# Kernel optimization log

Hardware: AMD Instinct MI355X
Metric: run time of the kernel (lower is better)

## Reference

```python
import jax, jax.numpy as jnp
from jax import lax
import numpy as np

INPUT, HIDDEN, OUTPUT, SEQ = 1024, 1024, 1024, 8192


def setup_inputs() -> dict:
    key = jax.random.key(0)
    ks = jax.random.split(key, 7)
    s = 1.0 / np.sqrt(HIDDEN)
    return {
        "input_seq": jax.random.normal(ks[0], (SEQ, INPUT), dtype=jnp.float32),
        # PyTorch nn.LSTM params, gate order [i, f, g, o]
        "W_ih": jax.random.uniform(ks[1], (4 * HIDDEN, INPUT), jnp.float32, -s, s),
        "W_hh": jax.random.uniform(ks[2], (4 * HIDDEN, HIDDEN), jnp.float32, -s, s),
        "b_ih": jax.random.uniform(ks[3], (4 * HIDDEN,), jnp.float32, -s, s),
        "b_hh": jax.random.uniform(ks[4], (4 * HIDDEN,), jnp.float32, -s, s),
        "W_out": jax.random.uniform(ks[5], (OUTPUT, HIDDEN), jnp.float32, -s, s),
        "b_out": jax.random.uniform(ks[6], (OUTPUT,), jnp.float32, -s, s),
    }


def reference(input_seq, W_ih, W_hh, b_ih, b_hh, W_out, b_out):
    H = W_hh.shape[1]
    # Precompute input projections for all timesteps in one GEMM: [S, 4H]
    x_gates = input_seq @ W_ih.T + (b_ih + b_hh)

    def step(carry, xg):
        h, c = carry
        gates = xg + h @ W_hh.T                      # [4H]
        i = jax.nn.sigmoid(gates[:H])
        f = jax.nn.sigmoid(gates[H:2 * H])
        g = jnp.tanh(gates[2 * H:3 * H])
        o = jax.nn.sigmoid(gates[3 * H:])
        c = f * c + i * g
        h = o * jnp.tanh(c)
        return (h, c), None

    h0 = jnp.zeros((H,), dtype=input_seq.dtype)
    (h_final, _), _ = lax.scan(step, (h0, h0), x_gates)
    # Original applies linear per-timestep then takes predictions[-1];
    # linear is pointwise in time, so projecting only h_final is identical math.
    return h_final @ W_out.T + b_out
```

## Files before the change

### kernel.cpp

```cpp
#include <hip/hip_runtime.h>
#include <hip/hip_fp16.h>

typedef _Float16 h2v __attribute__((ext_vector_type(2)));

__device__ __forceinline__ float fdot2(unsigned int a, unsigned int b, float c) {
    return __builtin_amdgcn_fdot2(__builtin_bit_cast(h2v, a),
                                  __builtin_bit_cast(h2v, b), c, false);
}

#define SCOPE_SYS __HIP_MEMORY_SCOPE_SYSTEM

__global__ __launch_bounds__(256) void k_f2h(const float* __restrict__ src,
                                             __half* __restrict__ dst, int n4) {
    int i = blockIdx.x * 256 + threadIdx.x;
    if (i >= n4) return;
    float4 v = ((const float4*)src)[i];
    union { __half2 h[2]; uint2 u; } o;
    o.h[0] = __halves2half2(__float2half_rn(v.x), __float2half_rn(v.y));
    o.h[1] = __halves2half2(__float2half_rn(v.z), __float2half_rn(v.w));
    ((uint2*)dst)[i] = o.u;
}

__global__ __launch_bounds__(256) void k_bias(const float* __restrict__ a,
                                              const float* __restrict__ b,
                                              float* __restrict__ o) {
    int i = blockIdx.x * 256 + threadIdx.x;
    if (i < 4096) o[i] = a[i] + b[i];
}

__global__ __launch_bounds__(256) void k_gemm_xg(const __half* __restrict__ A,
                                                 const __half* __restrict__ B,
                                                 const float* __restrict__ bias,
                                                 __half* __restrict__ C) {
    __shared__ unsigned int As[128][20];
    __shared__ unsigned int Bs[128][20];
    const int tid = threadIdx.x;
    const int tx = tid & 15, ty = tid >> 4;
    const int m0 = blockIdx.x * 128, n0 = blockIdx.y * 128;
    float acc[8][8];
#pragma unroll
    for (int i = 0; i < 8; ++i)
#pragma unroll
        for (int j = 0; j < 8; ++j) acc[i][j] = 0.f;
    const unsigned int* Ag = (const unsigned int*)(A + (size_t)m0 * 1024);
    const unsigned int* Bg = (const unsigned int*)(B + (size_t)n0 * 1024);
    for (int k0 = 0; k0 < 512; k0 += 16) {
        __syncthreads();
#pragma unroll
        for (int j = 0; j < 2; ++j) {
            int qd = j * 256 + tid;
            int row = qd >> 2;
            int c4 = (qd & 3) << 2;
            uint4 va = *(const uint4*)(Ag + (size_t)row * 512 + k0 + c4);
            uint4 vb = *(const uint4*)(Bg + (size_t)row * 512 + k0 + c4);
            *(uint4*)&As[row][c4] = va;
            *(uint4*)&Bs[row][c4] = vb;
        }
        __syncthreads();
#pragma unroll
        for (int k2 = 0; k2 < 16; k2 += 2) {
            unsigned int a0[8], a1[8], b0[8], b1[8];
#pragma unroll
            for (int i = 0; i < 8; ++i) {
                uint2 v = *(const uint2*)&As[ty + 16 * i][k2];
                a0[i] = v.x; a1[i] = v.y;
            }
#pragma unroll
            for (int j = 0; j < 8; ++j) {
                uint2 v = *(const uint2*)&Bs[tx + 16 * j][k2];
                b0[j] = v.x; b1[j] = v.y;
            }
#pragma unroll
            for (int i = 0; i < 8; ++i)
#pragma unroll
                for (int j = 0; j < 8; ++j) {
                    acc[i][j] = fdot2(a0[i], b0[j], acc[i][j]);
                    acc[i][j] = fdot2(a1[i], b1[j], acc[i][j]);
                }
        }
    }
#pragma unroll
    for (int i = 0; i < 8; ++i) {
        int row = m0 + ty + 16 * i;
#pragma unroll
        for (int j = 0; j < 8; ++j) {
            int col = n0 + tx + 16 * j;
            C[(size_t)row * 4096 + col] = __float2half_rn(acc[i][j] + bias[col]);
        }
    }
}

__global__ __launch_bounds__(512, 1) void k_lstm(const __half* __restrict__ Whh,
                                                 const __half* __restrict__ xg,
                                                 unsigned int* pub) {
    __shared__ uint4 Wp[18][512];
    __shared__ unsigned int hs[2][544];
    const int tid = threadIdx.x;
    const int b = blockIdx.x;
    const int w = tid >> 6, lane = tid & 63;
    const int rho = lane >> 2;
    const int cc = lane & 3;
    const int grow = (rho & 3) * 1024 + b * 32 + 4 * w + (rho >> 2);
    const unsigned int* gw = (const unsigned int*)(Whh + (size_t)grow * 1024 + cc * 256);
#pragma unroll
    for (int i = 0; i < 18; ++i)
        Wp[i][tid] = *(const uint4*)(gw + i * 4);
    const int soff = (tid >> 6) * 68 + (tid & 63);
    const int upub = b * 32 + w * 4 + (lane >> 4);
    float c_state = 0.f;
    __syncthreads();

    for (int t = 0; t < 8192; ++t) {
        uint4 pv[14];
#pragma unroll
        for (int i = 0; i < 14; ++i)
            pv[i] = *(const uint4*)(gw + (18 + i) * 4);
#pragma unroll
        for (int i = 0; i < 14; ++i)
            asm volatile("" : "+v"(pv[i].x), "+v"(pv[i].y), "+v"(pv[i].z), "+v"(pv[i].w));
        float xv = __half2float(xg[(size_t)t * 4096 + grow]);
        unsigned int d = 0;
        if (t > 0) {
            const unsigned long long* src =
                (const unsigned long long*)(pub + (((t - 1) & 1) << 10)) + tid;
            const unsigned tt = (unsigned)t;
            unsigned long long v = __hip_atomic_load(src, __ATOMIC_RELAXED, SCOPE_SYS);
            unsigned lo = (unsigned)v, hi = (unsigned)(v >> 32);
            while ((lo >> 16) != tt || (hi >> 16) != tt) {
                v = __hip_atomic_load(src, __ATOMIC_RELAXED, SCOPE_SYS);
                lo = (unsigned)v; hi = (unsigned)(v >> 32);
            }
            d = (lo & 0xffffu) | (hi << 16);
        }
        const int p = t & 1;
        hs[p][soff] = d;
        __syncthreads();
        float a0 = 0.f, a1 = 0.f, a2 = 0.f, a3 = 0.f;
        const unsigned int* hsp = &hs[p][cc * 136];
#pragma unroll
        for (int i = 0; i < 18; ++i) {
            uint4 wv = Wp[i][tid];
            uint4 h4 = *(const uint4*)(hsp + (i >> 4) * 68 + ((i & 15) << 2));
            a0 = fdot2(wv.x, h4.x, a0);
            a1 = fdot2(wv.y, h4.y, a1);
            a2 = fdot2(wv.z, h4.z, a2);
            a3 = fdot2(wv.w, h4.w, a3);
        }
#pragma unroll
        for (int i = 0; i < 14; ++i) {
            int s = 18 + i;
            uint4 h4 = *(const uint4*)(hsp + (s >> 4) * 68 + ((s & 15) << 2));
            a0 = fdot2(pv[i].x, h4.x, a0);
            a1 = fdot2(pv[i].y, h4.y, a1);
            a2 = fdot2(pv[i].z, h4.z, a2);
            a3 = fdot2(pv[i].w, h4.w, a3);
        }
        float acc = (a0 + a1) + (a2 + a3);
        acc += __shfl_xor(acc, 1);
        acc += __shfl_xor(acc, 2);
        acc += xv;
        const int base = lane & 48;
        float gi = __shfl(acc, base + 0);
        float gf = __shfl(acc, base + 4);
        float gg = __shfl(acc, base + 8);
        float go = __shfl(acc, base + 12);
        gi = 1.f / (1.f + __expf(-gi));
        gf = 1.f / (1.f + __expf(-gf));
        gg = 2.f / (1.f + __expf(-2.f * gg)) - 1.f;
        go = 1.f / (1.f + __expf(-go));
        c_state = gf * c_state + gi * gg;
        float hval = go * (2.f / (1.f + __expf(-2.f * c_state)) - 1.f);
        if ((lane & 15) == 0) {
            unsigned val = ((unsigned)(t + 1) << 16) |
                           (unsigned)__half_as_ushort(__float2half_rn(hval));
            __hip_atomic_store(pub + (p << 10) + upub, val,
                               __ATOMIC_RELAXED, SCOPE_SYS);
        }
    }
}

__global__ __launch_bounds__(256) void k_proj(const unsigned int* __restrict__ hfin,
                                              const float* __restrict__ Wout,
                                              const float* __restrict__ bout,
                                              float* __restrict__ out) {
    __shared__ float red[256];
    const int o = blockIdx.x, tid = threadIdx.x;
    const float* wr = Wout + (size_t)o * 1024;
    float acc = 0.f;
#pragma unroll
    for (int j = 0; j < 4; ++j) {
        int e = j * 256 + tid;
        unsigned v = hfin[e];
        acc += __half2float(__ushort_as_half((unsigned short)(v & 0xffffu))) * wr[e];
    }
    red[tid] = acc;
    __syncthreads();
    for (int s = 128; s > 0; s >>= 1) {
        if (tid < s) red[tid] += red[tid + s];
        __syncthreads();
    }
    if (tid == 0) out[o] = red[0] + bout[o];
}

extern "C" void kernel_launch(void* const* d_in, const int* in_sizes, int n_in,
                              void* d_out, int out_size, void* d_ws, size_t ws_size,
                              hipStream_t stream) {
    const float* input_seq = (const float*)d_in[0];
    const float* W_ih = (const float*)d_in[1];
    const float* W_hh = (const float*)d_in[2];
    const float* b_ih = (const float*)d_in[3];
    const float* b_hh = (const float*)d_in[4];
    const float* W_out = (const float*)d_in[5];
    const float* b_out = (const float*)d_in[6];
    float* out = (float*)d_out;

    char* ws = (char*)d_ws;
    unsigned int* pub = (unsigned int*)ws;
    float* bias = (float*)(ws + 24576);
    __half* Wih_h = (__half*)(ws + 65536);
    __half* Whh_h = (__half*)(ws + 65536 + (size_t)8 * 1024 * 1024);
    __half* in_h  = (__half*)(ws + 65536 + (size_t)16 * 1024 * 1024);
    __half* xg    = (__half*)(ws + 65536 + (size_t)32 * 1024 * 1024);

    hipMemsetAsync(ws, 0, 8192, stream);

    k_f2h<<<8192, 256, 0, stream>>>(input_seq, in_h, 2 * 1024 * 1024);
    k_f2h<<<4096, 256, 0, stream>>>(W_ih, Wih_h, 1024 * 1024);
    k_f2h<<<4096, 256, 0, stream>>>(W_hh, Whh_h, 1024 * 1024);
    k_bias<<<16, 256, 0, stream>>>(b_ih, b_hh, bias);

    dim3 gg(64, 32);
    k_gemm_xg<<<gg, 256, 0, stream>>>(in_h, Wih_h, bias, xg);

    k_lstm<<<32, 512, 0, stream>>>(Whh_h, xg, pub);

    k_proj<<<1024, 256, 0, stream>>>(pub + 1024, W_out, b_out, out);
}
```

Measured before the change: 17.38 ms.

## Remap LSTM recurrent work so each 16-lane group owns all four gates of a unit

The thread-to-weight mapping in the persistent LSTM kernel is reorganised. Each group of 16 threads now handles one hidden unit across all four gates, with each thread covering a 64-element slice of K. This replaces the per-gate row ownership that needed cross-lane shuffles to gather the i/f/g/o values. Each thread loads its hidden-state slice from LDS once into registers and reuses it for four gate accumulators. The cost is a longer 16-lane shuffle reduction per gate and four x-gate loads per step.

Result: slower. 18.14 ms (+4.4%).

```diff
diff --git a/kernel.cpp b/kernel.cpp
--- a/kernel.cpp
+++ b/kernel.cpp
@@ -94,31 +94,35 @@
                                                  const __half* __restrict__ xg,
                                                  unsigned int* pub) {
     __shared__ uint4 Wp[18][512];
-    __shared__ unsigned int hs[2][544];
+    __shared__ unsigned int hs[2][576];
     const int tid = threadIdx.x;
     const int b = blockIdx.x;
-    const int w = tid >> 6, lane = tid & 63;
-    const int rho = lane >> 2;
-    const int cc = lane & 3;
-    const int grow = (rho & 3) * 1024 + b * 32 + 4 * w + (rho >> 2);
-    const unsigned int* gw = (const unsigned int*)(Whh + (size_t)grow * 1024 + cc * 256);
-#pragma unroll
-    for (int i = 0; i < 18; ++i)
-        Wp[i][tid] = *(const uint4*)(gw + i * 4);
-    const int soff = (tid >> 6) * 68 + (tid & 63);
-    const int upub = b * 32 + w * 4 + (lane >> 4);
+    const int u = tid >> 4;
+    const int j = tid & 15;
+    const unsigned int* gw =
+        (const unsigned int*)(Whh + ((size_t)b * 32 + u) * 1024 + j * 64);
+#pragma unroll
+    for (int s = 0; s < 18; ++s)
+        Wp[s][tid] = *(const uint4*)(gw + (s >> 3) * 524288 + (s & 7) * 4);
+    const int soff = (tid >> 5) * 36 + (tid & 31);
+    const int upub = b * 32 + u;
     float c_state = 0.f;
     __syncthreads();
 
     for (int t = 0; t < 8192; ++t) {
         uint4 pv[14];
 #pragma unroll
-        for (int i = 0; i < 14; ++i)
-            pv[i] = *(const uint4*)(gw + (18 + i) * 4);
+        for (int i = 0; i < 14; ++i) {
+            int s = 18 + i;
+            pv[i] = *(const uint4*)(gw + (s >> 3) * 524288 + (s & 7) * 4);
+        }
+        float xv[4];
+#pragma unroll
+        for (int q = 0; q < 4; ++q)
+            xv[q] = __half2float(xg[(size_t)t * 4096 + q * 1024 + b * 32 + u]);
 #pragma unroll
         for (int i = 0; i < 14; ++i)
             asm volatile("" : "+v"(pv[i].x), "+v"(pv[i].y), "+v"(pv[i].z), "+v"(pv[i].w));
-        float xv = __half2float(xg[(size_t)t * 4096 + grow]);
         unsigned int d = 0;
         if (t > 0) {
             const unsigned long long* src =
@@ -135,42 +139,38 @@
         const int p = t & 1;
         hs[p][soff] = d;
         __syncthreads();
-        float a0 = 0.f, a1 = 0.f, a2 = 0.f, a3 = 0.f;
-        const unsigned int* hsp = &hs[p][cc * 136];
-#pragma unroll
-        for (int i = 0; i < 18; ++i) {
-            uint4 wv = Wp[i][tid];
-            uint4 h4 = *(const uint4*)(hsp + (i >> 4) * 68 + ((i & 15) << 2));
-            a0 = fdot2(wv.x, h4.x, a0);
-            a1 = fdot2(wv.y, h4.y, a1);
-            a2 = fdot2(wv.z, h4.z, a2);
-            a3 = fdot2(wv.w, h4.w, a3);
-        }
-#pragma unroll
-        for (int i = 0; i < 14; ++i) {
-            int s = 18 + i;
-            uint4 h4 = *(const uint4*)(hsp + (s >> 4) * 68 + ((s & 15) << 2));
-            a0 = fdot2(pv[i].x, h4.x, a0);
-            a1 = fdot2(pv[i].y, h4.y, a1);
-            a2 = fdot2(pv[i].z, h4.z, a2);
-            a3 = fdot2(pv[i].w, h4.w, a3);
-        }
-        float acc = (a0 + a1) + (a2 + a3);
-        acc += __shfl_xor(acc, 1);
-        acc += __shfl_xor(acc, 2);
-        acc += xv;
-        const int base = lane & 48;
-        float gi = __shfl(acc, base + 0);
-        float gf = __shfl(acc, base + 4);
-        float gg = __shfl(acc, base + 8);
-        float go = __shfl(acc, base + 12);
-        gi = 1.f / (1.f + __expf(-gi));
-        gf = 1.f / (1.f + __expf(-gf));
-        gg = 2.f / (1.f + __expf(-2.f * gg)) - 1.f;
-        go = 1.f / (1.f + __expf(-go));
+        const unsigned int* hsp = &hs[p][j * 36];
+        uint4 h4[8];
+#pragma unroll
+        for (int i = 0; i < 8; ++i)
+            h4[i] = *(const uint4*)(hsp + i * 4);
+        float acc[4] = {0.f, 0.f, 0.f, 0.f};
+#pragma unroll
+        for (int q = 0; q < 4; ++q)
+#pragma unroll
+            for (int i = 0; i < 8; ++i) {
+                int s = q * 8 + i;
+                uint4 wv = (s < 18) ? Wp[s][tid] : pv[s - 18];
+                acc[q] = fdot2(wv.x, h4[i].x, acc[q]);
+                acc[q] = fdot2(wv.y, h4[i].y, acc[q]);
+                acc[q] = fdot2(wv.z, h4[i].z, acc[q]);
+                acc[q] = fdot2(wv.w, h4[i].w, acc[q]);
+            }
+#pragma unroll
+        for (int q = 0; q < 4; ++q) {
+            acc[q] += __shfl_xor(acc[q], 1);
+            acc[q] += __shfl_xor(acc[q], 2);
+            acc[q] += __shfl_xor(acc[q], 4);
+            acc[q] += __shfl_xor(acc[q], 8);
+            acc[q] += xv[q];
+        }
+        float gi = 1.f / (1.f + __expf(-acc[0]));
+        float gf = 1.f / (1.f + __expf(-acc[1]));
+        float gg = 2.f / (1.f + __expf(-2.f * acc[2])) - 1.f;
+        float go = 1.f / (1.f + __expf(-acc[3]));
         c_state = gf * c_state + gi * gg;
         float hval = go * (2.f / (1.f + __expf(-2.f * c_state)) - 1.f);
-        if ((lane & 15) == 0) {
+        if (j == 0) {
             unsigned val = ((unsigned)(t + 1) << 16) |
                            (unsigned)__half_as_ushort(__float2half_rn(hval));
             __hip_atomic_store(pub + (p << 10) + upub, val,
```

## Pin LSTM workgroups to a single XCC and use agent-scope flag atomics

Applied to the files above, without the earlier changes.

Launches 256 LSTM workgroups and has each read its hardware XCC id. The first XCC to gather 32 workgroups wins; its workgroups take slots 0-31 and all others exit. The per-step hidden-state publish/poll atomics drop from system to agent scope. The aim is to keep the cross-workgroup exchange inside one XCC's L2 and cut the cost of each of the 8192 serial handoffs. The risk is that the winning XCC cannot hold 32 co-resident workgroups, which would deadlock, and that agent-scope coherence across XCCs is relied on only implicitly.

Measured after the change: 19.07 ms. 9.7% more time.

```diff
diff --git a/kernel.cpp b/kernel.cpp
--- a/kernel.cpp
+++ b/kernel.cpp
@@ -8,7 +8,8 @@
                                   __builtin_bit_cast(h2v, b), c, false);
 }
 
-#define SCOPE_SYS __HIP_MEMORY_SCOPE_SYSTEM
+#define SCOPE_AGENT __HIP_MEMORY_SCOPE_AGENT
+#define SCOPE_SYS   __HIP_MEMORY_SCOPE_SYSTEM
 
 __global__ __launch_bounds__(256) void k_f2h(const float* __restrict__ src,
                                              __half* __restrict__ dst, int n4) {
@@ -92,11 +93,31 @@
 
 __global__ __launch_bounds__(512, 1) void k_lstm(const __half* __restrict__ Whh,
                                                  const __half* __restrict__ xg,
-                                                 unsigned int* pub) {
+                                                 unsigned int* pub,
+                                                 int* ctl) {
     __shared__ uint4 Wp[18][512];
     __shared__ unsigned int hs[2][544];
+    __shared__ int sslot;
     const int tid = threadIdx.x;
-    const int b = blockIdx.x;
+
+    if (tid == 0) {
+        unsigned xcc;
+        asm volatile("s_getreg_b32 %0, hwreg(HW_REG_XCC_ID)" : "=s"(xcc));
+        int slot = -1;
+        int idx = atomicAdd(&ctl[xcc], 1);
+        if (idx < 32) {
+            if (idx == 31) atomicCAS(&ctl[8], 0, (int)xcc + 1);
+            int win;
+            while ((win = __hip_atomic_load(&ctl[8], __ATOMIC_RELAXED, SCOPE_SYS)) == 0)
+                __builtin_amdgcn_s_sleep(8);
+            if (win == (int)xcc + 1) slot = idx;
+        }
+        sslot = slot;
+    }
+    __syncthreads();
+    const int b = sslot;
+    if (b < 0) return;
+
     const int w = tid >> 6, lane = tid & 63;
     const int rho = lane >> 2;
     const int cc = lane & 3;
@@ -124,10 +145,10 @@
             const unsigned long long* src =
                 (const unsigned long long*)(pub + (((t - 1) & 1) << 10)) + tid;
             const unsigned tt = (unsigned)t;
-            unsigned long long v = __hip_atomic_load(src, __ATOMIC_RELAXED, SCOPE_SYS);
+            unsigned long long v = __hip_atomic_load(src, __ATOMIC_RELAXED, SCOPE_AGENT);
             unsigned lo = (unsigned)v, hi = (unsigned)(v >> 32);
             while ((lo >> 16) != tt || (hi >> 16) != tt) {
-                v = __hip_atomic_load(src, __ATOMIC_RELAXED, SCOPE_SYS);
+                v = __hip_atomic_load(src, __ATOMIC_RELAXED, SCOPE_AGENT);
                 lo = (unsigned)v; hi = (unsigned)(v >> 32);
             }
             d = (lo & 0xffffu) | (hi << 16);
@@ -174,7 +195,7 @@
             unsigned val = ((unsigned)(t + 1) << 16) |
                            (unsigned)__half_as_ushort(__float2half_rn(hval));
             __hip_atomic_store(pub + (p << 10) + upub, val,
-                               __ATOMIC_RELAXED, SCOPE_SYS);
+                               __ATOMIC_RELAXED, SCOPE_AGENT);
         }
     }
 }
@@ -216,13 +237,14 @@
 
     char* ws = (char*)d_ws;
     unsigned int* pub = (unsigned int*)ws;
+    int* ctl = (int*)(ws + 8192);
     float* bias = (float*)(ws + 24576);
     __half* Wih_h = (__half*)(ws + 65536);
     __half* Whh_h = (__half*)(ws + 65536 + (size_t)8 * 1024 * 1024);
     __half* in_h  = (__half*)(ws + 65536 + (size_t)16 * 1024 * 1024);
     __half* xg    = (__half*)(ws + 65536 + (size_t)32 * 1024 * 1024);
 
-    hipMemsetAsync(ws, 0, 8192, stream);
+    hipMemsetAsync(ws, 0, 8320, stream);
 
     k_f2h<<<8192, 256, 0, stream>>>(input_seq, in_h, 2 * 1024 * 1024);
     k_f2h<<<4096, 256, 0, stream>>>(W_ih, Wih_h, 1024 * 1024);
@@ -232,7 +254,7 @@
     dim3 gg(64, 32);
     k_gemm_xg<<<gg, 256, 0, stream>>>(in_h, Wih_h, bias, xg);
 
-    k_lstm<<<32, 512, 0, stream>>>(Whh_h, xg, pub);
+    k_lstm<<<256, 512, 0, stream>>>(Whh_h, xg, pub, ctl);
 
     k_proj<<<1024, 256, 0, stream>>>(pub + 1024, W_out, b_out, out);
 }
```
